# Kernel tuning notes

Hardware: AMD Instinct MI355X
Metric: run time of the kernel (lower is better)

Reference implementation:

```python
import math
import jax, jax.numpy as jnp
import numpy as np

EPS = 1e-5
KS = 8          # emb_ks == emb_hs
NH = 4          # attention heads
LOOKBACK = 5
NLAYERS = 4


def prelu(x, a):
    return jnp.where(x >= 0, x, a * x)


def ln_c(x, g, b):
    # LayerNormalization4D: stats over channel dim; note (std + eps) denominator
    mu = jnp.mean(x, 1, keepdims=True)
    var = jnp.mean((x - mu) ** 2, 1, keepdims=True)
    return (x - mu) / (jnp.sqrt(var + EPS) + EPS) * g[None, :, None, None] + b[None, :, None, None]


def ln_cf_head(x, g, b):
    # x: [H, B, E, T, F]; stats over (E, F); g, b: [H, E, F]
    mu = jnp.mean(x, (2, 4), keepdims=True)
    var = jnp.mean((x - mu) ** 2, (2, 4), keepdims=True)
    return (x - mu) / (jnp.sqrt(var + EPS) + EPS) * g[:, None, :, None, :] + b[:, None, :, None, :]


def ln_cf_proj(x, g, b):
    # x: [B, C, T, F]; stats over (C, F); g, b: [C, F]
    mu = jnp.mean(x, (1, 3), keepdims=True)
    var = jnp.mean((x - mu) ** 2, (1, 3), keepdims=True)
    return (x - mu) / (jnp.sqrt(var + EPS) + EPS) * g[None, :, None, :] + b[None, :, None, :]


def lstm(x, wih, whh, bih, bhh):
    # x: [N, T, I] -> hidden sequence [N, T, H]; PyTorch gate order i, f, g, o
    xp = jnp.einsum('nti,gi->ntg', x, wih) + bih + bhh
    H = whh.shape[1]
    N = x.shape[0]

    def step(carry, xt):
        h, c = carry
        gates = xt + h @ whh.T
        i, f, g, o = jnp.split(gates, 4, axis=-1)
        c = jax.nn.sigmoid(f) * c + jax.nn.sigmoid(i) * jnp.tanh(g)
        h = jax.nn.sigmoid(o) * jnp.tanh(c)
        return (h, c), h

    init = (jnp.zeros((N, H), x.dtype), jnp.zeros((N, H), x.dtype))
    _, hs = jax.lax.scan(step, init, jnp.swapaxes(xp, 0, 1))
    return jnp.swapaxes(hs, 0, 1)


def bilstm(x, wih, whh, bih, bhh):
    fwd = lstm(x, wih[0], whh[0], bih[0], bhh[0])
    bwd = lstm(x[:, ::-1], wih[1], whh[1], bih[1], bhh[1])[:, ::-1]
    return jnp.concatenate([fwd, bwd], -1)


def unfold1d(x):
    # non-overlapping unfold (ks == stride == KS): [N, C, L] -> [N, L//KS, C*KS]
    N, C, Lx = x.shape
    return x.reshape(N, C, Lx // KS, KS).transpose(0, 2, 1, 3).reshape(N, Lx // KS, C * KS)


def fold1d(h, w, b):
    # ConvTranspose1d with stride == kernel == KS; h: [N, Lp, D], w: [D, C, KS]
    y = jnp.einsum('nld,dck->nlck', h, w)
    N, Lp, C, K = y.shape
    return y.transpose(0, 2, 1, 3).reshape(N, C, Lp * K) + b[None, :, None]


def conv2d(x, w, b):
    y = jax.lax.conv_general_dilated(x, w, (1, 1), ((1, 1), (1, 1)),
                                     dimension_numbers=('NCHW', 'OIHW', 'NCHW'))
    return y + b[None, :, None, None]


def block(x, p):
    B, C, oT, oF = x.shape
    T = math.ceil((oT - KS) / KS) * KS + KS
    F = math.ceil((oF - KS) / KS) * KS + KS
    x = jnp.pad(x, ((0, 0), (0, 0), (0, T - oT), (0, F - oF)))
    input_ = x
    # intra (frequency) bidirectional LSTM
    z = ln_c(input_, p['intra_norm_g'], p['intra_norm_b'])
    z = z.transpose(0, 2, 1, 3).reshape(B * T, C, F)
    z = unfold1d(z)                                    # [B*T, F//KS, C*KS]
    h = bilstm(z, p['intra_wih'], p['intra_whh'], p['intra_bih'], p['intra_bhh'])
    z = fold1d(h, p['intra_lin_w'], p['intra_lin_b'])  # [B*T, C, F]
    intra = z.reshape(B, T, C, F).transpose(0, 2, 1, 3) + input_
    # inter (time) causal LSTM
    z = ln_c(intra, p['inter_norm_g'], p['inter_norm_b'])
    z = z.transpose(0, 3, 1, 2).reshape(B * F, C, T)
    z = unfold1d(z)                                    # [B*F, T//KS, C*KS]
    h = lstm(z, p['inter_wih'], p['inter_whh'], p['inter_bih'], p['inter_bhh'])
    z = fold1d(h, p['inter_lin_w'], p['inter_lin_b'])  # [B*F, C, T]
    inter = z.reshape(B, F, C, T).transpose(0, 2, 3, 1) + intra
    inter = inter[..., :oT, :oF]

    # per-head 1x1-conv QKV (batched over heads) + local causal attention
    def qkv(w, b, a, g, beta):
        y = jnp.einsum('bctf,hec->hbetf', inter, w) + b[:, None, :, None, None]
        y = prelu(y, a[:, None, None, None, None])
        return ln_cf_head(y, g, beta)

    Q = qkv(p['q_w'], p['q_b'], p['q_a'], p['q_g'], p['q_beta'])
    K = qkv(p['k_w'], p['k_b'], p['k_a'], p['k_g'], p['k_beta'])
    V = qkv(p['v_w'], p['v_b'], p['v_a'], p['v_g'], p['v_beta'])
    E = Q.shape[2]
    CV = V.shape[2]
    Qf = Q.transpose(0, 1, 3, 2, 4).reshape(NH, B, oT, E * oF)
    Kf = K.transpose(0, 1, 3, 2, 4).reshape(NH, B, oT, E * oF)
    Vf = V.transpose(0, 1, 3, 2, 4).reshape(NH, B, oT, CV * oF)
    attn = jnp.einsum('hbtd,hbsd->hbts', Qf, Kf) / jnp.sqrt(jnp.asarray(E * oF, Qf.dtype))
    t = jnp.arange(oT)
    d = t[:, None] - t[None, :]
    mask = (d >= 0) & (d <= LOOKBACK)      # causal with 5-frame lookback
    attn = jnp.where(mask, attn, -1e30)
    A = jax.nn.softmax(attn, axis=-1)
    O = jnp.einsum('hbts,hbsd->hbtd', A, Vf).reshape(NH, B, oT, CV, oF)
    O = O.transpose(1, 0, 3, 2, 4).reshape(B, NH * CV, oT, oF)
    y = jnp.einsum('bctf,dc->bdtf', O, p['proj_w']) + p['proj_b'][None, :, None, None]
    y = prelu(y, p['proj_a'])
    y = ln_cf_proj(y, p['proj_g'], p['proj_beta'])
    return y + inter


def _forward(x, conv_w, conv_b, gn_g, gn_b,
             intra_norm_g, intra_norm_b, intra_wih, intra_whh, intra_bih, intra_bhh,
             intra_lin_w, intra_lin_b,
             inter_norm_g, inter_norm_b, inter_wih, inter_whh, inter_bih, inter_bhh,
             inter_lin_w, inter_lin_b,
             q_w, q_b, q_a, q_g, q_beta,
             k_w, k_b, k_a, k_g, k_beta,
             v_w, v_b, v_a, v_g, v_beta,
             proj_w, proj_b, proj_a, proj_g, proj_beta,
             deconv_w, deconv_b):
    esti = conv2d(x, conv_w, conv_b)
    # GroupNorm(1, emb_dim): per-sample stats over (C, T, F), per-channel affine
    mu = jnp.mean(esti, (1, 2, 3), keepdims=True)
    var = jnp.mean((esti - mu) ** 2, (1, 2, 3), keepdims=True)
    esti = (esti - mu) / jnp.sqrt(var + EPS) * gn_g[None, :, None, None] + gn_b[None, :, None, None]
    stacked = dict(
        intra_norm_g=intra_norm_g, intra_norm_b=intra_norm_b,
        intra_wih=intra_wih, intra_whh=intra_whh, intra_bih=intra_bih, intra_bhh=intra_bhh,
        intra_lin_w=intra_lin_w, intra_lin_b=intra_lin_b,
        inter_norm_g=inter_norm_g, inter_norm_b=inter_norm_b,
        inter_wih=inter_wih, inter_whh=inter_whh, inter_bih=inter_bih, inter_bhh=inter_bhh,
        inter_lin_w=inter_lin_w, inter_lin_b=inter_lin_b,
        q_w=q_w, q_b=q_b, q_a=q_a, q_g=q_g, q_beta=q_beta,
        k_w=k_w, k_b=k_b, k_a=k_a, k_g=k_g, k_beta=k_beta,
        v_w=v_w, v_b=v_b, v_a=v_a, v_g=v_g, v_beta=v_beta,
        proj_w=proj_w, proj_b=proj_b, proj_a=proj_a, proj_g=proj_g, proj_beta=proj_beta,
    )
    for l in range(NLAYERS):
        p = {k: v[l] for k, v in stacked.items()}
        esti = block(esti, p)
    # ConvTranspose2d(k=3, s=1, p=1) == conv with spatially flipped, io-swapped kernel, pad 1
    w2 = jnp.flip(deconv_w, (2, 3)).transpose(1, 0, 2, 3)
    return conv2d(esti, w2, deconv_b)


def setup_inputs() -> dict:
    key = jax.random.key(0)
    keys = iter(jax.random.split(key, 80))

    def rn(shape, s=0.05):
        return jax.random.normal(next(keys), shape, jnp.float32) * s

    L, C, H, E, CV, FA = 4, 32, 256, 4, 8, 161
    IN = C * KS
    return dict(
        x=jax.random.normal(next(keys), (8, 2, 504, 161), jnp.float32),
        conv_w=rn((C, 2, 3, 3)), conv_b=jnp.zeros((C,), jnp.float32),
        gn_g=jnp.ones((C,), jnp.float32), gn_b=jnp.zeros((C,), jnp.float32),
        intra_norm_g=jnp.ones((L, C), jnp.float32), intra_norm_b=jnp.zeros((L, C), jnp.float32),
        intra_wih=rn((L, 2, 4 * H, IN)), intra_whh=rn((L, 2, 4 * H, H)),
        intra_bih=jnp.zeros((L, 2, 4 * H), jnp.float32), intra_bhh=jnp.zeros((L, 2, 4 * H), jnp.float32),
        intra_lin_w=rn((L, 2 * H, C, KS)), intra_lin_b=jnp.zeros((L, C), jnp.float32),
        inter_norm_g=jnp.ones((L, C), jnp.float32), inter_norm_b=jnp.zeros((L, C), jnp.float32),
        inter_wih=rn((L, 4 * H, IN)), inter_whh=rn((L, 4 * H, H)),
        inter_bih=jnp.zeros((L, 4 * H), jnp.float32), inter_bhh=jnp.zeros((L, 4 * H), jnp.float32),
        inter_lin_w=rn((L, H, C, KS)), inter_lin_b=jnp.zeros((L, C), jnp.float32),
        q_w=rn((L, NH, E, C)), q_b=jnp.zeros((L, NH, E), jnp.float32),
        q_a=jnp.full((L, NH), 0.25, jnp.float32),
        q_g=jnp.ones((L, NH, E, FA), jnp.float32), q_beta=jnp.zeros((L, NH, E, FA), jnp.float32),
        k_w=rn((L, NH, E, C)), k_b=jnp.zeros((L, NH, E), jnp.float32),
        k_a=jnp.full((L, NH), 0.25, jnp.float32),
        k_g=jnp.ones((L, NH, E, FA), jnp.float32), k_beta=jnp.zeros((L, NH, E, FA), jnp.float32),
        v_w=rn((L, NH, CV, C)), v_b=jnp.zeros((L, NH, CV), jnp.float32),
        v_a=jnp.full((L, NH), 0.25, jnp.float32),
        v_g=jnp.ones((L, NH, CV, FA), jnp.float32), v_beta=jnp.zeros((L, NH, CV, FA), jnp.float32),
        proj_w=rn((L, C, C)), proj_b=jnp.zeros((L, C), jnp.float32),
        proj_a=jnp.full((L,), 0.25, jnp.float32),
        proj_g=jnp.ones((L, C, FA), jnp.float32), proj_beta=jnp.zeros((L, C, FA), jnp.float32),
        deconv_w=rn((C, 2, 3, 3)), deconv_b=jnp.zeros((2,), jnp.float32),
    )


def reference(x, conv_w, conv_b, gn_g, gn_b,
              intra_norm_g, intra_norm_b, intra_wih, intra_whh, intra_bih, intra_bhh,
              intra_lin_w, intra_lin_b,
              inter_norm_g, inter_norm_b, inter_wih, inter_whh, inter_bih, inter_bhh,
              inter_lin_w, inter_lin_b,
              q_w, q_b, q_a, q_g, q_beta,
              k_w, k_b, k_a, k_g, k_beta,
              v_w, v_b, v_a, v_g, v_beta,
              proj_w, proj_b, proj_a, proj_g, proj_beta,
              deconv_w, deconv_b):
    return _forward(x, conv_w, conv_b, gn_g, gn_b,
                    intra_norm_g, intra_norm_b, intra_wih, intra_whh, intra_bih, intra_bhh,
                    intra_lin_w, intra_lin_b,
                    inter_norm_g, inter_norm_b, inter_wih, inter_whh, inter_bih, inter_bhh,
                    inter_lin_w, inter_lin_b,
                    q_w, q_b, q_a, q_g, q_beta,
                    k_w, k_b, k_a, k_g, k_beta,
                    v_w, v_b, v_a, v_g, v_beta,
                    proj_w, proj_b, proj_a, proj_g, proj_beta,
                    deconv_w, deconv_b)
```

## Files before the change

kernel.cpp:

```cpp
#include <hip/hip_runtime.h>
#include <hip/hip_bf16.h>
#include <math.h>

#define BB   8
#define CH   32
#define TT   504
#define FFp  168
#define OF   161
#define KSZ  8
#define HID  256
#define NG   1024
#define NHh  4
#define EE   4
#define CVv  8
#define N1   4032
#define N2   1344
#define LFi  21
#define LTi  63
#define EPSf 1e-5f

#define AS1 __attribute__((address_space(1)))
#define AS3 __attribute__((address_space(3)))

typedef __hip_bfloat16 bf16;
typedef __attribute__((ext_vector_type(8))) short s16x8;
typedef __attribute__((ext_vector_type(4))) float f32x4;

__device__ __forceinline__ float b2f(bf16 v) { return __bfloat162float(v); }
__device__ __forceinline__ bf16 f2b(float v) { return __float2bfloat16(v); }
__device__ __forceinline__ float us2f(unsigned short u) {
  return __uint_as_float(((unsigned)u) << 16);
}
__device__ __forceinline__ unsigned short f2bu(float v) {
  unsigned u = __float_as_uint(v);
  unsigned r = u + 0x7fffu + ((u >> 16) & 1u);
  return (unsigned short)(r >> 16);
}

__device__ __forceinline__ float sigm(float x) { return 1.f / (1.f + __expf(-x)); }
__device__ __forceinline__ float tanh_f(float x) {
  x = fminf(15.f, fmaxf(-15.f, x));
  float e = __expf(2.f * x);
  return (e - 1.f) / (e + 1.f);
}

__device__ __forceinline__ void block_reduce2(float& s1, float& s2, float* red) {
#pragma unroll
  for (int off = 32; off > 0; off >>= 1) {
    s1 += __shfl_down(s1, off, 64);
    s2 += __shfl_down(s2, off, 64);
  }
  int lane = threadIdx.x & 63, wv = threadIdx.x >> 6;
  __syncthreads();
  if (lane == 0) { red[wv * 2] = s1; red[wv * 2 + 1] = s2; }
  __syncthreads();
  s1 = red[0] + red[2] + red[4] + red[6];
  s2 = red[1] + red[3] + red[5] + red[7];
}

__global__ __launch_bounds__(192) void conv_in_k(const float* __restrict__ x,
                                                 const float* __restrict__ w,
                                                 const float* __restrict__ bias,
                                                 bf16* __restrict__ out) {
  __shared__ float xs[2 * 3 * (OF + 3)];
  int bt = blockIdx.x;
  int b = bt / TT, t = bt % TT;
  int tid = threadIdx.x;
  for (int i = tid; i < 2 * 3 * (OF + 3); i += 192) {
    int ci = i / (3 * (OF + 3));
    int rem = i % (3 * (OF + 3));
    int rr = rem / (OF + 3);
    int f = rem % (OF + 3);
    int ts = t + rr - 1;
    float v = 0.f;
    if (ts >= 0 && ts < TT && f < OF) v = x[((size_t)(b * 2 + ci) * TT + ts) * OF + f];
    xs[i] = v;
  }
  __syncthreads();
  int f = tid;
  if (f < OF) {
    float xv[2][3][3];
#pragma unroll
    for (int ci = 0; ci < 2; ci++)
#pragma unroll
      for (int kh = 0; kh < 3; kh++)
#pragma unroll
        for (int kw = 0; kw < 3; kw++) {
          int ff = f + kw - 1;
          xv[ci][kh][kw] = (ff < 0) ? 0.f : xs[(ci * 3 + kh) * (OF + 3) + ff];
        }
    for (int co = 0; co < CH; co++) {
      float acc = bias[co];
#pragma unroll
      for (int ci = 0; ci < 2; ci++)
#pragma unroll
        for (int kh = 0; kh < 3; kh++)
#pragma unroll
          for (int kw = 0; kw < 3; kw++)
            acc += xv[ci][kh][kw] * w[((co * 2 + ci) * 3 + kh) * 3 + kw];
      out[((size_t)(b * CH + co) * TT + t) * OF + f] = f2b(acc);
    }
  }
}

__global__ __launch_bounds__(256) void gn_reduce_k(const bf16* __restrict__ xin,
                                                   float* __restrict__ stats) {
  const int M = CH * TT * OF;
  int b = blockIdx.x >> 6;
  int part = blockIdx.x & 63;
  const bf16* p = xin + (size_t)b * M;
  float s1 = 0.f, s2 = 0.f;
  for (int i = part * 256 + threadIdx.x; i < M; i += 64 * 256) {
    float v = b2f(p[i]);
    s1 += v; s2 += v * v;
  }
  __shared__ float red[8];
  block_reduce2(s1, s2, red);
  if (threadIdx.x == 0) {
    atomicAdd(&stats[b * 2], s1);
    atomicAdd(&stats[b * 2 + 1], s2);
  }
}

__global__ __launch_bounds__(256) void gn_apply_k(const bf16* __restrict__ xin,
                                                  const float* __restrict__ stats,
                                                  const float* __restrict__ g,
                                                  const float* __restrict__ bb,
                                                  bf16* __restrict__ act) {
  int gid = blockIdx.x * 256 + threadIdx.x;
  int f = gid % FFp;
  int t = (gid / FFp) % TT;
  int c = (gid / (FFp * TT)) % CH;
  int b = gid / (FFp * TT * CH);
  float v = 0.f;
  if (f < OF) {
    const float M = (float)(CH * TT * OF);
    float mu = stats[b * 2] / M;
    float var = stats[b * 2 + 1] / M - mu * mu;
    float xv = b2f(xin[((size_t)(b * CH + c) * TT + t) * OF + f]);
    v = (xv - mu) * rsqrtf(var + EPSf) * g[c] + bb[c];
  }
  act[gid] = f2b(v);
}

__global__ __launch_bounds__(256) void ln_unfold_k(const bf16* __restrict__ xin,
                                                   const float* __restrict__ g,
                                                   const float* __restrict__ bb,
                                                   bf16* __restrict__ out) {
  __shared__ float sm[CH * FFp];
  __shared__ float mu_s[FFp], rs_s[FFp];
  __shared__ float gg[CH], bv[CH];
  int bt = blockIdx.x;
  int b = bt / TT, t = bt % TT;
  int tid = threadIdx.x;
  if (tid < CH) { gg[tid] = g[tid]; bv[tid] = bb[tid]; }
  const bf16* base = xin + ((size_t)b * CH * TT + t) * FFp;
  for (int idx = tid; idx < CH * FFp; idx += 256) {
    int c = idx / FFp, f = idx % FFp;
    sm[idx] = b2f(base[(size_t)c * TT * FFp + f]);
  }
  __syncthreads();
  if (tid < FFp) {
    int f = tid;
    float s1 = 0.f, s2 = 0.f;
#pragma unroll
    for (int c = 0; c < CH; c++) { float v = sm[c * FFp + f]; s1 += v; s2 += v * v; }
    float mu = s1 / CH;
    float var = s2 / CH - mu * mu;
    mu_s[f] = mu;
    rs_s[f] = 1.f / (sqrtf(var + EPSf) + EPSf);
  }
  __syncthreads();
  unsigned short* outu = (unsigned short*)out;
  for (int ch = tid; ch < LFi * CH; ch += 256) {
    int gI = ch >> 5, c = ch & 31;
    float gc = gg[c], bc = bv[c];
    unsigned short o8[8];
#pragma unroll
    for (int k = 0; k < 8; k++) {
      int f = gI * 8 + k;
      float v = (sm[c * FFp + f] - mu_s[f]) * rs_s[f] * gc + bc;
      o8[k] = f2bu(v);
    }
    *(uint4*)(outu + ((size_t)gI * N1 + bt) * 256 + c * 8) = *(uint4*)o8;
  }
}

__global__ __launch_bounds__(256) void ln_unfold8_k(const bf16* __restrict__ xin,
                                                    const float* __restrict__ g,
                                                    const float* __restrict__ bb,
                                                    bf16* __restrict__ out) {
  __shared__ short smb[8 * CH * FFp];
  __shared__ float mu_s[8 * FFp], rs_s[8 * FFp];
  __shared__ float gg[CH], bv[CH];
  int tg = blockIdx.x, b = blockIdx.y;
  int tid = threadIdx.x;
  if (tid < CH) { gg[tid] = g[tid]; bv[tid] = bb[tid]; }
  const short* src = (const short*)xin;
  for (int idx = tid; idx < 8 * CH * (FFp / 8); idx += 256) {
    int t8 = idx / (CH * 21);
    int rem = idx % (CH * 21);
    int c = rem / 21, fc = rem % 21;
    s16x8 v = *(const s16x8*)(src + ((size_t)(b * CH + c) * TT + tg * 8 + t8) * FFp + fc * 8);
    *(s16x8*)(&smb[(t8 * CH + c) * FFp + fc * 8]) = v;
  }
  __syncthreads();
  for (int p = tid; p < 8 * FFp; p += 256) {
    int t8 = p / FFp, f = p % FFp;
    float s1 = 0.f, s2 = 0.f;
#pragma unroll
    for (int c = 0; c < CH; c++) {
      float v = us2f((unsigned short)smb[(t8 * CH + c) * FFp + f]);
      s1 += v; s2 += v * v;
    }
    float mu = s1 / CH;
    float var = s2 / CH - mu * mu;
    mu_s[p] = mu;
    rs_s[p] = 1.f / (sqrtf(var + EPSf) + EPSf);
  }
  __syncthreads();
  unsigned short* outu = (unsigned short*)out;
  for (int ch = tid; ch < FFp * CH; ch += 256) {
    int f = ch >> 5, c = ch & 31;
    float gc = gg[c], bc = bv[c];
    unsigned short o8[8];
#pragma unroll
    for (int k = 0; k < 8; k++) {
      float v = us2f((unsigned short)smb[(k * CH + c) * FFp + f]);
      v = (v - mu_s[k * FFp + f]) * rs_s[k * FFp + f] * gc + bc;
      o8[k] = f2bu(v);
    }
    *(uint4*)(outu + ((size_t)tg * N2 + b * FFp + f) * 256 + c * 8) = *(uint4*)o8;
  }
}

__global__ __launch_bounds__(256) void lstm_prep_k(const float* __restrict__ wih0,
                                                   const float* __restrict__ whh0,
                                                   bf16* __restrict__ blob0) {
  int dir = blockIdx.y;
  const float* wih = wih0 + (size_t)dir * 262144;
  const float* whh = whh0 + (size_t)dir * 262144;
  unsigned short* blob = (unsigned short*)(blob0 + (size_t)dir * 524288);
  int gid = blockIdx.x * 256 + threadIdx.x;
  int lane = gid & 63;
  int ks = (gid >> 6) & 15;
  int nt = gid >> 10;
  int n = nt * 16 + (lane & 15);
  int kb = ks * 32 + (lane >> 4) * 8;
  unsigned short o8[8];
#pragma unroll
  for (int j = 0; j < 8; j++) {
    int k = kb + j;
    float v = (k < 256) ? wih[n * 256 + k] : whh[n * 256 + (k - 256)];
    o8[j] = f2bu(v);
  }
  *(uint4*)(blob + (size_t)gid * 8) = *(uint4*)o8;
}

__global__ __launch_bounds__(512) void lstm_mfma_k(const bf16* __restrict__ xz,
                                                   const bf16* __restrict__ blob0,
                                                   const float* __restrict__ bih0,
                                                   const float* __restrict__ bhh0,
                                                   bf16* __restrict__ hout,
                                                   int N, int Ls, int hstride, int bidir) {
  __shared__ __attribute__((aligned(16))) short afr[16 * 2 * 64 * 8];
  extern __shared__ __attribute__((aligned(16))) short bstage[];
  int tid = threadIdx.x;
  int w = tid >> 6, lane = tid & 63;
  int l15 = lane & 15, lq = lane >> 4;
  int dir = blockIdx.y;
  const short* blob = (const short*)(blob0 + (size_t)dir * 524288);
  const float* bih = bih0 + dir * NG;
  const float* bhh = bhh0 + dir * NG;
  int hoff = dir * 256;
  int n0 = blockIdx.x * 32;
  unsigned short* houtu = (unsigned short*)hout;
  const short* xzs = (const short*)xz;
  short* bst_w = bstage + w * 4096;

  float bias[4][2];
#pragma unroll
  for (int q = 0; q < 4; q++)
#pragma unroll
    for (int j = 0; j < 2; j++) {
      int n = q * 256 + (2 * w + j) * 16 + l15;
      bias[q][j] = bih[n] + bhh[n];
    }
  for (int i = tid; i < 8192; i += 512) afr[8192 + i] = 0;
  float cst[16];
#pragma unroll
  for (int i = 0; i < 16; i++) cst[i] = 0.f;

#define BQ_ISSUE(C)                                                              \
  {                                                                              \
    int c32_ = (C) >> 1, h2_ = (C) & 1;                                          \
    int a_ = c32_ >> 3, r_ = c32_ & 7;                                           \
    int nt_ = (r_ >> 1) * 16 + 2 * w + (r_ & 1);                                 \
    const short* gb_ = blob + (size_t)nt_ * 8192 + (a_ * 4 + h2_ * 2) * 512 + lane * 8; \
    short* lb_ = bst_w + ((C) & 3) * 1024;                                       \
    _Pragma("unroll")                                                            \
    for (int k_ = 0; k_ < 2; k_++)                                               \
      __builtin_amdgcn_global_load_lds((const AS1 void*)(gb_ + k_ * 512),        \
                                       (AS3 void*)(lb_ + k_ * 512), 16, 0, 0);   \
  }

  for (int st = 0; st < Ls; st++) {
    int t = (bidir && dir) ? (Ls - 1 - st) : st;
    {
      const short* gx = xzs + ((size_t)t * N + n0 + l15) * 256 + (w * 4 + lq) * 8;
      __builtin_amdgcn_global_load_lds((const AS1 void*)gx,
                                       (AS3 void*)(afr + (w * 2 + 0) * 512), 16, 0, 0);
      __builtin_amdgcn_global_load_lds((const AS1 void*)(gx + 16 * 256),
                                       (AS3 void*)(afr + (w * 2 + 1) * 512), 16, 0, 0);
    }
    BQ_ISSUE(0);
    BQ_ISSUE(1);
    BQ_ISSUE(2);
    __syncthreads();

    f32x4 acc[2][4][2];
#pragma unroll
    for (int mt = 0; mt < 2; mt++)
#pragma unroll
      for (int q = 0; q < 4; q++)
#pragma unroll
        for (int j = 0; j < 2; j++)
          acc[mt][q][j] = (f32x4){bias[q][j], bias[q][j], bias[q][j], bias[q][j]};

    s16x8 af[4][2];
#pragma unroll
    for (int C = 0; C < 64; C++) {
      int c32 = C >> 1, h2 = C & 1;
      int rR = c32 & 7;
      int q = rR >> 1, j = rR & 1;
      if (rR == 0 && h2 == 0) {
        int a = c32 >> 3;
#pragma unroll
        for (int k = 0; k < 4; k++)
#pragma unroll
          for (int mt = 0; mt < 2; mt++)
            af[k][mt] = *(const s16x8*)(&afr[(((a * 4 + k) * 2 + mt) * 64 + lane) * 8]);
      }
      if (C < 62)       __builtin_amdgcn_s_waitcnt(0x0F74);
      else if (C == 62) __builtin_amdgcn_s_waitcnt(0x0F72);
      else              __builtin_amdgcn_s_waitcnt(0x0F70);
      const short* lb = bst_w + (C & 3) * 1024;
#pragma unroll
      for (int k = 0; k < 2; k++) {
        s16x8 bf = *(const s16x8*)(lb + k * 512 + lane * 8);
        acc[0][q][j] = __builtin_amdgcn_mfma_f32_16x16x32_bf16(af[h2 * 2 + k][0], bf, acc[0][q][j], 0, 0, 0);
        acc[1][q][j] = __builtin_amdgcn_mfma_f32_16x16x32_bf16(af[h2 * 2 + k][1], bf, acc[1][q][j], 0, 0, 0);
      }
      if (C < 61) BQ_ISSUE(C + 3);
    }
    __syncthreads();

#pragma unroll
    for (int mt = 0; mt < 2; mt++)
#pragma unroll
      for (int j = 0; j < 2; j++) {
        int d = (2 * w + j) * 16 + l15;
        int slotb = ((8 + (d >> 5)) * 2 + mt) * 64 + ((d >> 3) & 3) * 16;
#pragma unroll
        for (int r = 0; r < 4; r++) {
          int m = lq * 4 + r;
          float iv = sigm(acc[mt][0][j][r]);
          float fv = sigm(acc[mt][1][j][r]);
          float gv = tanh_f(acc[mt][2][j][r]);
          float ov = sigm(acc[mt][3][j][r]);
          float c = fv * cst[mt * 8 + j * 4 + r] + iv * gv;
          cst[mt * 8 + j * 4 + r] = c;
          float h = ov * tanh_f(c);
          unsigned short hb = f2bu(h);
          houtu[((size_t)t * N + n0 + mt * 16 + m) * hstride + hoff + d] = hb;
          afr[(slotb + m) * 8 + (d & 7)] = (short)hb;
        }
      }
  }
#undef BQ_ISSUE
}

__global__ __launch_bounds__(256) void fold_gemm_k(const bf16* __restrict__ A,
                                                   const float* __restrict__ Bw,
                                                   const float* __restrict__ linb,
                                                   const bf16* __restrict__ resid,
                                                   bf16* __restrict__ outp,
                                                   int K, int mode) {
  __shared__ float As[16 * 68];
  __shared__ float Bs[16 * 64];
  int tid = threadIdx.x;
  int n0 = blockIdx.x * 64;
  int m0 = blockIdx.y * 64;
  int tr = tid >> 4, tc = tid & 15;
  float acc[4][4] = {};
  int arow = tid >> 2, akg = (tid & 3) * 4;
  int bkk = tid >> 4, bc4 = (tid & 15) * 4;
  for (int k0 = 0; k0 < K; k0 += 16) {
    ushort4 avu = *(const ushort4*)((const unsigned short*)A + (size_t)(m0 + arow) * K + k0 + akg);
    float4 bv = *(const float4*)(Bw + (size_t)(k0 + bkk) * 256 + n0 + bc4);
    __syncthreads();
    As[(akg + 0) * 68 + arow] = us2f(avu.x);
    As[(akg + 1) * 68 + arow] = us2f(avu.y);
    As[(akg + 2) * 68 + arow] = us2f(avu.z);
    As[(akg + 3) * 68 + arow] = us2f(avu.w);
    *(float4*)(&Bs[bkk * 64 + bc4]) = bv;
    __syncthreads();
#pragma unroll
    for (int kk = 0; kk < 16; kk++) {
      float4 a4 = *(const float4*)(&As[kk * 68 + tr * 4]);
      float4 b4 = *(const float4*)(&Bs[kk * 64 + tc * 4]);
      float aa[4] = {a4.x, a4.y, a4.z, a4.w};
      float bb_[4] = {b4.x, b4.y, b4.z, b4.w};
#pragma unroll
      for (int i = 0; i < 4; i++)
#pragma unroll
        for (int j = 0; j < 4; j++) acc[i][j] += aa[i] * bb_[j];
    }
  }
#pragma unroll
  for (int i = 0; i < 4; i++) {
    int r = m0 + tr * 4 + i;
#pragma unroll
    for (int j = 0; j < 4; j++) {
      int col = n0 + tc * 4 + j;
      int c = col >> 3, kp = col & 7;
      float v = acc[i][j] + linb[c];
      if (mode == 0) {
        int l = r / N1, n = r % N1;
        int b = n / TT, t = n % TT;
        size_t o = ((size_t)(b * CH + c) * TT + t) * FFp + (l * 8 + kp);
        outp[o] = f2b(v + b2f(resid[o]));
      } else {
        int l = r / N2, n = r % N2;
        int b = n / FFp, fq = n % FFp;
        int t = l * 8 + kp;
        if (fq < OF) {
          size_t o = ((size_t)(b * CH + c) * TT + t) * OF + fq;
          size_t ri = ((size_t)(b * CH + c) * TT + t) * FFp + fq;
          outp[o] = f2b(v + b2f(resid[ri]));
        }
      }
    }
  }
}

__global__ __launch_bounds__(256) void qkv_k(const bf16* __restrict__ interc,
    const float* __restrict__ qw, const float* __restrict__ qb, const float* __restrict__ qa,
    const float* __restrict__ qg, const float* __restrict__ qbeta,
    const float* __restrict__ kw, const float* __restrict__ kb, const float* __restrict__ ka,
    const float* __restrict__ kg, const float* __restrict__ kbeta,
    const float* __restrict__ vw, const float* __restrict__ vb, const float* __restrict__ va,
    const float* __restrict__ vg, const float* __restrict__ vbeta,
    bf16* __restrict__ qo, bf16* __restrict__ ko, bf16* __restrict__ vo) {
  __shared__ float sm[CH * OF];
  __shared__ float wb[16 * 32];
  __shared__ float wbias[16];
  __shared__ float yb[16 * OF];
  __shared__ float red[8];
  int bt = blockIdx.x, h = blockIdx.y;
  int b = bt / TT, t = bt % TT;
  int tid = threadIdx.x;
  const bf16* src = interc + ((size_t)b * CH * TT + t) * OF;
  for (int idx = tid; idx < CH * OF; idx += 256) {
    int c = idx / OF, f = idx % OF;
    sm[idx] = b2f(src[(size_t)c * TT * OF + f]);
  }
  for (int idx = tid; idx < 512; idx += 256) {
    int e = idx >> 5, c = idx & 31;
    float w;
    if (e < 4) w = qw[(h * 4 + e) * 32 + c];
    else if (e < 8) w = kw[(h * 4 + e - 4) * 32 + c];
    else w = vw[(h * 8 + e - 8) * 32 + c];
    wb[idx] = w;
  }
  if (tid < 16) {
    float bv;
    if (tid < 4) bv = qb[h * 4 + tid];
    else if (tid < 8) bv = kb[h * 4 + tid - 4];
    else bv = vb[h * 8 + tid - 8];
    wbias[tid] = bv;
  }
  __syncthreads();
  float aQ = qa[h], aK = ka[h], aV = va[h];
  for (int idx = tid; idx < 16 * OF; idx += 256) {
    int e = idx / OF, f = idx % OF;
    float accv = wbias[e];
#pragma unroll
    for (int c = 0; c < 32; c++) accv += sm[c * OF + f] * wb[e * 32 + c];
    float a = e < 4 ? aQ : (e < 8 ? aK : aV);
    yb[idx] = accv >= 0.f ? accv : a * accv;
  }
  __syncthreads();
  for (int seg = 0; seg < 3; seg++) {
    int s0 = (seg == 0) ? 0 : ((seg == 1) ? 644 : 1288);
    int len = (seg == 2) ? 1288 : 644;
    float s1 = 0.f, s2 = 0.f;
    for (int i = tid; i < len; i += 256) { float v = yb[s0 + i]; s1 += v; s2 += v * v; }
    block_reduce2(s1, s2, red);
    float mu = s1 / len;
    float var = s2 / len - mu * mu;
    float rs = 1.f / (sqrtf(var + EPSf) + EPSf);
    const float* gp; const float* bp; bf16* op; int nch;
    if (seg == 0) { gp = qg; bp = qbeta; op = qo; nch = 4; }
    else if (seg == 1) { gp = kg; bp = kbeta; op = ko; nch = 4; }
    else { gp = vg; bp = vbeta; op = vo; nch = 8; }
    for (int i = tid; i < len; i += 256) {
      int e = i / OF, f = i % OF;
      float v = (yb[s0 + i] - mu) * rs * gp[(h * nch + e) * OF + f] + bp[(h * nch + e) * OF + f];
      op[(((size_t)(h * BB + b) * nch + e) * TT + t) * OF + f] = f2b(v);
    }
  }
}

__global__ __launch_bounds__(256) void attn_k(const bf16* __restrict__ Q,
                                              const bf16* __restrict__ Kt,
                                              const bf16* __restrict__ V,
                                              bf16* __restrict__ O) {
  int t = blockIdx.x;
  int hb = blockIdx.y;
  int h = hb >> 3, b = hb & 7;
  int tid = threadIdx.x;
  int nv = min(t, 5) + 1;
  const float scale = 0.0394055201f;
  __shared__ float redl[24];
  float part[6] = {0, 0, 0, 0, 0, 0};
  size_t qkbase = ((size_t)(h * BB + b) * EE) * TT * OF;
  for (int i = tid; i < EE * OF; i += 256) {
    int e = i / OF, f = i % OF;
    float qv = b2f(Q[qkbase + ((size_t)e * TT + t) * OF + f]);
#pragma unroll
    for (int d = 0; d < 6; d++)
      if (d < nv) part[d] += qv * b2f(Kt[qkbase + ((size_t)e * TT + (t - d)) * OF + f]);
  }
#pragma unroll
  for (int d = 0; d < 6; d++)
#pragma unroll
    for (int off = 32; off > 0; off >>= 1) part[d] += __shfl_down(part[d], off, 64);
  int lane = tid & 63, wv = tid >> 6;
  if (lane == 0) {
#pragma unroll
    for (int d = 0; d < 6; d++) redl[wv * 6 + d] = part[d];
  }
  __syncthreads();
  float a[6], sv[6];
  float m = -1e30f;
#pragma unroll
  for (int d = 0; d < 6; d++)
    if (d < nv) {
      float s = (redl[d] + redl[6 + d] + redl[12 + d] + redl[18 + d]) * scale;
      sv[d] = s;
      m = fmaxf(m, s);
    }
  float denom = 0.f;
#pragma unroll
  for (int d = 0; d < 6; d++)
    if (d < nv) { a[d] = __expf(sv[d] - m); denom += a[d]; }
  float inv = 1.f / denom;
  size_t vbase = ((size_t)(h * BB + b) * CVv) * TT * OF;
  for (int i = tid; i < CVv * OF; i += 256) {
    int cv = i / OF, f = i % OF;
    float o = 0.f;
#pragma unroll
    for (int d = 0; d < 6; d++)
      if (d < nv) o += a[d] * b2f(V[vbase + ((size_t)cv * TT + (t - d)) * OF + f]);
    O[(((size_t)b * CH + h * CVv + cv) * TT + t) * OF + f] = f2b(o * inv);
  }
}

__global__ __launch_bounds__(256) void proj_k(const bf16* __restrict__ ob,
                                              const float* __restrict__ pw,
                                              const float* __restrict__ pb,
                                              const float* __restrict__ pa,
                                              const float* __restrict__ pg,
                                              const float* __restrict__ pbeta,
                                              const bf16* __restrict__ interc,
                                              bf16* __restrict__ act) {
  __shared__ float sm[CH * OF];
  __shared__ float wsm[CH * CH];
  __shared__ float yb[CH * OF];
  __shared__ float red[8];
  int bt = blockIdx.x;
  int b = bt / TT, t = bt % TT;
  int tid = threadIdx.x;
  const bf16* src = ob + ((size_t)b * CH * TT + t) * OF;
  for (int idx = tid; idx < CH * OF; idx += 256) {
    int c = idx / OF, f = idx % OF;
    sm[idx] = b2f(src[(size_t)c * TT * OF + f]);
  }
  for (int idx = tid; idx < CH * CH; idx += 256) wsm[idx] = pw[idx];
  __syncthreads();
  float aP = pa[0];
  for (int idx = tid; idx < CH * OF; idx += 256) {
    int d = idx / OF, f = idx % OF;
    float accv = pb[d];
#pragma unroll
    for (int c = 0; c < 32; c++) accv += sm[c * OF + f] * wsm[d * 32 + c];
    yb[idx] = accv >= 0.f ? accv : aP * accv;
  }
  __syncthreads();
  float s1 = 0.f, s2 = 0.f;
  for (int i = tid; i < CH * OF; i += 256) { float v = yb[i]; s1 += v; s2 += v * v; }
  block_reduce2(s1, s2, red);
  const float Mn = (float)(CH * OF);
  float mu = s1 / Mn;
  float var = s2 / Mn - mu * mu;
  float rs = 1.f / (sqrtf(var + EPSf) + EPSf);
  for (int idx = tid; idx < CH * FFp; idx += 256) {
    int d = idx / FFp, f = idx % FFp;
    float v = 0.f;
    if (f < OF) {
      float y = (yb[d * OF + f] - mu) * rs * pg[d * OF + f] + pbeta[d * OF + f];
      v = y + b2f(interc[((size_t)(b * CH + d) * TT + t) * OF + f]);
    }
    act[((size_t)(b * CH + d) * TT + t) * FFp + f] = f2b(v);
  }
}

__global__ __launch_bounds__(256) void deconv_k(const bf16* __restrict__ act,
                                                const float* __restrict__ w,
                                                const float* __restrict__ bias,
                                                float* __restrict__ out) {
  __shared__ float ash[CH * 3 * FFp];
  int bt = blockIdx.x;
  int b = bt / TT, t = bt % TT;
  int tid = threadIdx.x;
  const short* acts = (const short*)act;
  for (int ch = tid; ch < CH * 3 * (FFp / 8); ch += 256) {
    int ci = ch / 63, rem = ch % 63;
    int rr = rem / 21, fc = rem % 21;
    int ts = t + rr - 1;
    float* dst = &ash[(ci * 3 + rr) * FFp + fc * 8];
    if (ts < 0 || ts >= TT) {
#pragma unroll
      for (int k2 = 0; k2 < 8; k2++) dst[k2] = 0.f;
    } else {
      s16x8 v = *(const s16x8*)(acts + ((size_t)(b * CH + ci) * TT + ts) * FFp + fc * 8);
#pragma unroll
      for (int k2 = 0; k2 < 8; k2++) dst[k2] = us2f((unsigned short)v[k2]);
    }
  }
  __syncthreads();
  int f = tid;
  if (f < OF) {
    float acc0 = bias[0], acc1 = bias[1];
#pragma unroll 4
    for (int ci = 0; ci < CH; ci++) {
      const float* row = &ash[ci * 3 * FFp];
      float xv[3][3];
#pragma unroll
      for (int kh = 0; kh < 3; kh++)
#pragma unroll
        for (int kw = 0; kw < 3; kw++) {
          int ff = f + kw - 1;
          xv[kh][kw] = (ff < 0) ? 0.f : row[kh * FFp + ff];
        }
#pragma unroll
      for (int kh = 0; kh < 3; kh++)
#pragma unroll
        for (int kw = 0; kw < 3; kw++) {
          acc0 += xv[kh][kw] * w[((ci * 2 + 0) * 3 + (2 - kh)) * 3 + (2 - kw)];
          acc1 += xv[kh][kw] * w[((ci * 2 + 1) * 3 + (2 - kh)) * 3 + (2 - kw)];
        }
    }
    out[((size_t)(b * 2 + 0) * TT + t) * OF + f] = acc0;
    out[((size_t)(b * 2 + 1) * TT + t) * OF + f] = acc1;
  }
}

extern "C" void kernel_launch(void* const* d_in, const int* in_sizes, int n_in,
                              void* d_out, int out_size, void* d_ws, size_t ws_size,
                              hipStream_t stream) {
  const float* x            = (const float*)d_in[0];
  const float* conv_w       = (const float*)d_in[1];
  const float* conv_b       = (const float*)d_in[2];
  const float* gn_g         = (const float*)d_in[3];
  const float* gn_b         = (const float*)d_in[4];
  const float* intra_norm_g = (const float*)d_in[5];
  const float* intra_norm_b = (const float*)d_in[6];
  const float* intra_wih    = (const float*)d_in[7];
  const float* intra_whh    = (const float*)d_in[8];
  const float* intra_bih    = (const float*)d_in[9];
  const float* intra_bhh    = (const float*)d_in[10];
  const float* intra_lin_w  = (const float*)d_in[11];
  const float* intra_lin_b  = (const float*)d_in[12];
  const float* inter_norm_g = (const float*)d_in[13];
  const float* inter_norm_b = (const float*)d_in[14];
  const float* inter_wih    = (const float*)d_in[15];
  const float* inter_whh    = (const float*)d_in[16];
  const float* inter_bih    = (const float*)d_in[17];
  const float* inter_bhh    = (const float*)d_in[18];
  const float* inter_lin_w  = (const float*)d_in[19];
  const float* inter_lin_b  = (const float*)d_in[20];
  const float* q_w    = (const float*)d_in[21];
  const float* q_b    = (const float*)d_in[22];
  const float* q_a    = (const float*)d_in[23];
  const float* q_g    = (const float*)d_in[24];
  const float* q_beta = (const float*)d_in[25];
  const float* k_w    = (const float*)d_in[26];
  const float* k_b    = (const float*)d_in[27];
  const float* k_a    = (const float*)d_in[28];
  const float* k_g    = (const float*)d_in[29];
  const float* k_beta = (const float*)d_in[30];
  const float* v_w    = (const float*)d_in[31];
  const float* v_b    = (const float*)d_in[32];
  const float* v_a    = (const float*)d_in[33];
  const float* v_g    = (const float*)d_in[34];
  const float* v_beta = (const float*)d_in[35];
  const float* proj_w    = (const float*)d_in[36];
  const float* proj_b    = (const float*)d_in[37];
  const float* proj_a    = (const float*)d_in[38];
  const float* proj_g    = (const float*)d_in[39];
  const float* proj_beta = (const float*)d_in[40];
  const float* deconv_w  = (const float*)d_in[41];
  const float* deconv_b  = (const float*)d_in[42];

  float* stats = (float*)d_ws;
  bf16* arena  = (bf16*)((char*)d_ws + 256);
  bf16* act    = arena;
  bf16* tmp    = arena + 21676032;
  bf16* hbuf   = arena + 43352064;
  bf16* res    = arena + 86704128;
  bf16* interc = arena + 108380160;
  bf16* convout = interc;
  bf16* qbuf = act;
  bf16* kbuf = tmp;
  bf16* vbuf = res;
  bf16* obuf = hbuf;
  bf16* blob_intra = res;
  bf16* blob_inter = interc;

  hipMemsetAsync(stats, 0, 64 * sizeof(float), stream);
  conv_in_k<<<4032, 192, 0, stream>>>(x, conv_w, conv_b, convout);
  gn_reduce_k<<<512, 256, 0, stream>>>(convout, stats);
  gn_apply_k<<<84672, 256, 0, stream>>>(convout, stats, gn_g, gn_b, act);

  for (int l = 0; l < 4; l++) {
    lstm_prep_k<<<dim3(256, 2), 256, 0, stream>>>(
        intra_wih + (size_t)l * 524288, intra_whh + (size_t)l * 524288, blob_intra);
    ln_unfold_k<<<4032, 256, 0, stream>>>(act, intra_norm_g + l * 32, intra_norm_b + l * 32, tmp);
    lstm_mfma_k<<<dim3(126, 2), 512, 65536, stream>>>(
        tmp, blob_intra, intra_bih + l * 2048, intra_bhh + l * 2048, hbuf, N1, LFi, 512, 1);
    fold_gemm_k<<<dim3(4, 1323), 256, 0, stream>>>(
        hbuf, intra_lin_w + (size_t)l * 131072, intra_lin_b + l * 32, act, res, 512, 0);
    lstm_prep_k<<<dim3(256, 1), 256, 0, stream>>>(
        inter_wih + (size_t)l * 262144, inter_whh + (size_t)l * 262144, blob_inter);
    ln_unfold8_k<<<dim3(LTi, BB), 256, 0, stream>>>(res, inter_norm_g + l * 32, inter_norm_b + l * 32, tmp);
    lstm_mfma_k<<<dim3(42, 1), 512, 65536, stream>>>(
        tmp, blob_inter, inter_bih + l * 1024, inter_bhh + l * 1024, hbuf, N2, LTi, 256, 0);
    fold_gemm_k<<<dim3(4, 1323), 256, 0, stream>>>(
        hbuf, inter_lin_w + (size_t)l * 65536, inter_lin_b + l * 32, res, interc, 256, 1);
    qkv_k<<<dim3(4032, 4), 256, 0, stream>>>(interc,
        q_w + l * 512, q_b + l * 16, q_a + l * 4, q_g + l * 2576, q_beta + l * 2576,
        k_w + l * 512, k_b + l * 16, k_a + l * 4, k_g + l * 2576, k_beta + l * 2576,
        v_w + l * 1024, v_b + l * 32, v_a + l * 4, v_g + l * 5152, v_beta + l * 5152,
        qbuf, kbuf, vbuf);
    attn_k<<<dim3(504, 32), 256, 0, stream>>>(qbuf, kbuf, vbuf, obuf);
    proj_k<<<4032, 256, 0, stream>>>(obuf, proj_w + l * 1024, proj_b + l * 32, proj_a + l,
                                     proj_g + l * 5152, proj_beta + l * 5152, interc, act);
  }
  deconv_k<<<4032, 256, 0, stream>>>(act, deconv_w, deconv_b, (float*)d_out);
}
```

Measured before the change: 15.92 ms.

## Deepen LSTM weight prefetch pipeline and stagger K-chunk order across blocks

```diff
diff --git a/kernel.cpp b/kernel.cpp
--- a/kernel.cpp
+++ b/kernel.cpp
@@ -257,26 +257,18 @@
   *(uint4*)(blob + (size_t)gid * 8) = *(uint4*)o8;
 }
 
-__global__ __launch_bounds__(512) void lstm_mfma_k(const bf16* __restrict__ xz,
-                                                   const bf16* __restrict__ blob0,
-                                                   const float* __restrict__ bih0,
-                                                   const float* __restrict__ bhh0,
-                                                   bf16* __restrict__ hout,
-                                                   int N, int Ls, int hstride, int bidir) {
-  __shared__ __attribute__((aligned(16))) short afr[16 * 2 * 64 * 8];
-  extern __shared__ __attribute__((aligned(16))) short bstage[];
-  int tid = threadIdx.x;
-  int w = tid >> 6, lane = tid & 63;
+template<int PH>
+__device__ __forceinline__ void lstm_run(short* __restrict__ afr,
+                                         short* __restrict__ bst_w,
+                                         const short* __restrict__ xzs,
+                                         const short* __restrict__ blob,
+                                         const float* __restrict__ bih,
+                                         const float* __restrict__ bhh,
+                                         unsigned short* __restrict__ houtu,
+                                         int N, int Ls, int hstride, int hoff,
+                                         int n0, int dirrev, int w, int lane) {
+  int tid = w * 64 + lane;
   int l15 = lane & 15, lq = lane >> 4;
-  int dir = blockIdx.y;
-  const short* blob = (const short*)(blob0 + (size_t)dir * 524288);
-  const float* bih = bih0 + dir * NG;
-  const float* bhh = bhh0 + dir * NG;
-  int hoff = dir * 256;
-  int n0 = blockIdx.x * 32;
-  unsigned short* houtu = (unsigned short*)hout;
-  const short* xzs = (const short*)xz;
-  short* bst_w = bstage + w * 4096;
 
   float bias[4][2];
 #pragma unroll
@@ -291,13 +283,13 @@
 #pragma unroll
   for (int i = 0; i < 16; i++) cst[i] = 0.f;
 
-#define BQ_ISSUE(C)                                                              \
+#define BQ_ISSUE(P)                                                              \
   {                                                                              \
-    int c32_ = (C) >> 1, h2_ = (C) & 1;                                          \
-    int a_ = c32_ >> 3, r_ = c32_ & 7;                                           \
-    int nt_ = (r_ >> 1) * 16 + 2 * w + (r_ & 1);                                 \
+    const int a_ = (((P) >> 4) + PH) & 3;                                        \
+    const int r_ = ((P) >> 1) & 7, h2_ = (P) & 1;                                \
+    const int nt_ = (r_ >> 1) * 16 + 2 * w + (r_ & 1);                           \
     const short* gb_ = blob + (size_t)nt_ * 8192 + (a_ * 4 + h2_ * 2) * 512 + lane * 8; \
-    short* lb_ = bst_w + ((C) & 3) * 1024;                                       \
+    short* lb_ = bst_w + ((P) % 6) * 1024;                                       \
     _Pragma("unroll")                                                            \
     for (int k_ = 0; k_ < 2; k_++)                                               \
       __builtin_amdgcn_global_load_lds((const AS1 void*)(gb_ + k_ * 512),        \
@@ -305,17 +297,19 @@
   }
 
   for (int st = 0; st < Ls; st++) {
-    int t = (bidir && dir) ? (Ls - 1 - st) : st;
+    int t = dirrev ? (Ls - 1 - st) : st;
     {
       const short* gx = xzs + ((size_t)t * N + n0 + l15) * 256 + (w * 4 + lq) * 8;
       __builtin_amdgcn_global_load_lds((const AS1 void*)gx,
-                                       (AS3 void*)(afr + (w * 2 + 0) * 512), 16, 0, 0);
+                                       (AS3 void*)(afr + (w * 2 + 0) * 512), 16, 0, 2);
       __builtin_amdgcn_global_load_lds((const AS1 void*)(gx + 16 * 256),
-                                       (AS3 void*)(afr + (w * 2 + 1) * 512), 16, 0, 0);
+                                       (AS3 void*)(afr + (w * 2 + 1) * 512), 16, 0, 2);
     }
     BQ_ISSUE(0);
     BQ_ISSUE(1);
     BQ_ISSUE(2);
+    BQ_ISSUE(3);
+    BQ_ISSUE(4);
     __syncthreads();
 
     f32x4 acc[2][4][2];
@@ -330,28 +324,30 @@
     s16x8 af[4][2];
 #pragma unroll
     for (int C = 0; C < 64; C++) {
-      int c32 = C >> 1, h2 = C & 1;
-      int rR = c32 & 7;
-      int q = rR >> 1, j = rR & 1;
+      const int s = C >> 1, h2 = C & 1;
+      const int rR = s & 7;
+      const int q = rR >> 1, j = rR & 1;
       if (rR == 0 && h2 == 0) {
-        int a = c32 >> 3;
+        const int a = ((s >> 3) + PH) & 3;
 #pragma unroll
         for (int k = 0; k < 4; k++)
 #pragma unroll
           for (int mt = 0; mt < 2; mt++)
             af[k][mt] = *(const s16x8*)(&afr[(((a * 4 + k) * 2 + mt) * 64 + lane) * 8]);
       }
-      if (C < 62)       __builtin_amdgcn_s_waitcnt(0x0F74);
+      if (C <= 59)      __builtin_amdgcn_s_waitcnt(0x0F78);
+      else if (C == 60) __builtin_amdgcn_s_waitcnt(0x0F76);
+      else if (C == 61) __builtin_amdgcn_s_waitcnt(0x0F74);
       else if (C == 62) __builtin_amdgcn_s_waitcnt(0x0F72);
       else              __builtin_amdgcn_s_waitcnt(0x0F70);
-      const short* lb = bst_w + (C & 3) * 1024;
+      const short* lb = bst_w + (C % 6) * 1024;
 #pragma unroll
       for (int k = 0; k < 2; k++) {
         s16x8 bf = *(const s16x8*)(lb + k * 512 + lane * 8);
         acc[0][q][j] = __builtin_amdgcn_mfma_f32_16x16x32_bf16(af[h2 * 2 + k][0], bf, acc[0][q][j], 0, 0, 0);
         acc[1][q][j] = __builtin_amdgcn_mfma_f32_16x16x32_bf16(af[h2 * 2 + k][1], bf, acc[1][q][j], 0, 0, 0);
       }
-      if (C < 61) BQ_ISSUE(C + 3);
+      if (C < 59) BQ_ISSUE(C + 5);
     }
     __syncthreads();
 
@@ -378,6 +374,35 @@
       }
   }
 #undef BQ_ISSUE
+}
+
+__global__ __launch_bounds__(512) void lstm_mfma_k(const bf16* __restrict__ xz,
+                                                   const bf16* __restrict__ blob0,
+                                                   const float* __restrict__ bih0,
+                                                   const float* __restrict__ bhh0,
+                                                   bf16* __restrict__ hout,
+                                                   int N, int Ls, int hstride, int bidir) {
+  __shared__ __attribute__((aligned(16))) short afr[16 * 2 * 64 * 8];
+  __shared__ __attribute__((aligned(16))) short bstage[8 * 6 * 1024];
+  int tid = threadIdx.x;
+  int w = tid >> 6, lane = tid & 63;
+  int dir = blockIdx.y;
+  const short* blob = (const short*)(blob0 + (size_t)dir * 524288);
+  const float* bih = bih0 + dir * NG;
+  const float* bhh = bhh0 + dir * NG;
+  int hoff = dir * 256;
+  int n0 = blockIdx.x * 32;
+  int dirrev = (bidir && dir) ? 1 : 0;
+  unsigned short* houtu = (unsigned short*)hout;
+  const short* xzs = (const short*)xz;
+  short* bst_w = bstage + w * 6144;
+  int PH = ((blockIdx.x >> 3) + blockIdx.x) & 3;
+  switch (PH) {
+    case 0: lstm_run<0>(afr, bst_w, xzs, blob, bih, bhh, houtu, N, Ls, hstride, hoff, n0, dirrev, w, lane); break;
+    case 1: lstm_run<1>(afr, bst_w, xzs, blob, bih, bhh, houtu, N, Ls, hstride, hoff, n0, dirrev, w, lane); break;
+    case 2: lstm_run<2>(afr, bst_w, xzs, blob, bih, bhh, houtu, N, Ls, hstride, hoff, n0, dirrev, w, lane); break;
+    default: lstm_run<3>(afr, bst_w, xzs, blob, bih, bhh, houtu, N, Ls, hstride, hoff, n0, dirrev, w, lane); break;
+  }
 }
 
 __global__ __launch_bounds__(256) void fold_gemm_k(const bf16* __restrict__ A,
@@ -738,14 +763,14 @@
     lstm_prep_k<<<dim3(256, 2), 256, 0, stream>>>(
         intra_wih + (size_t)l * 524288, intra_whh + (size_t)l * 524288, blob_intra);
     ln_unfold_k<<<4032, 256, 0, stream>>>(act, intra_norm_g + l * 32, intra_norm_b + l * 32, tmp);
-    lstm_mfma_k<<<dim3(126, 2), 512, 65536, stream>>>(
+    lstm_mfma_k<<<dim3(126, 2), 512, 0, stream>>>(
         tmp, blob_intra, intra_bih + l * 2048, intra_bhh + l * 2048, hbuf, N1, LFi, 512, 1);
     fold_gemm_k<<<dim3(4, 1323), 256, 0, stream>>>(
         hbuf, intra_lin_w + (size_t)l * 131072, intra_lin_b + l * 32, act, res, 512, 0);
     lstm_prep_k<<<dim3(256, 1), 256, 0, stream>>>(
         inter_wih + (size_t)l * 262144, inter_whh + (size_t)l * 262144, blob_inter);
     ln_unfold8_k<<<dim3(LTi, BB), 256, 0, stream>>>(res, inter_norm_g + l * 32, inter_norm_b + l * 32, tmp);
-    lstm_mfma_k<<<dim3(42, 1), 512, 65536, stream>>>(
+    lstm_mfma_k<<<dim3(42, 1), 512, 0, stream>>>(
         tmp, blob_inter, inter_bih + l * 1024, inter_bhh + l * 1024, hbuf, N2, LTi, 256, 0);
     fold_gemm_k<<<dim3(4, 1323), 256, 0, stream>>>(
         hbuf, inter_lin_w + (size_t)l * 65536, inter_lin_b + l * 32, res, interc, 256, 1);
```

New measurement: 15.13 ms. 1.05x faster.
